# Optimization experiments

Hardware: AMD Instinct MI355X
Metric: run time of the kernel (lower is better)

The kernel has to match this reference:

```python
import jax, jax.numpy as jnp
import numpy as np

B, L, D, H = 2, 2048, 1024, 16
HD = D // H  # head_dim = 64


def setup_inputs() -> dict:
    key = jax.random.key(0)
    k1, k2, k3, k4, k5 = jax.random.split(key, 5)
    s = 1.0 / np.sqrt(D)
    return {
        "x": jax.random.normal(k1, (B, L, D), dtype=jnp.float32),
        "quantum_scores": jax.random.normal(k2, (B, L, L), dtype=jnp.float32),
        "wq": jax.random.normal(k3, (D, D), dtype=jnp.float32) * s,
        "wk": jax.random.normal(k4, (D, D), dtype=jnp.float32) * s,
        "wv": jax.random.normal(k5, (D, D), dtype=jnp.float32) * s,
        "scale": jnp.ones((H, 1, 1), dtype=jnp.float32),
    }


def reference(x, quantum_scores, wq, wk, wv, scale):
    Bq, Lq, _ = x.shape
    # nn.Linear: y = x @ W^T ; then split heads -> (B, H, L, HD)
    def split_heads(t):
        return t.reshape(Bq, Lq, H, HD).transpose(0, 2, 1, 3)

    q = split_heads(x @ wq.T)
    k = split_heads(x @ wk.T)
    v = split_heads(x @ wv.T)

    logits = jnp.einsum("bhqd,bhkd->bhqk", q, k) / np.sqrt(HD).astype(np.float32)
    logits = logits + quantum_scores[:, None, :, :]          # quantum bias, broadcast over heads
    logits = logits * scale[None, :, :, :]                   # per-head learnable scale
    attn = jax.nn.softmax(logits, axis=-1)
    out = jnp.einsum("bhqk,bhkd->bhqd", attn, v)
    return out.transpose(0, 2, 1, 3).reshape(Bq, Lq, D)
```

## Files before the change

### kernel.cpp

```cpp
#include <hip/hip_runtime.h>

#define Bq 2
#define Lq 2048
#define Dq 1024
#define Hq 16
#define HDq 64

typedef _Float16 f16;
typedef _Float16 f16x8 __attribute__((ext_vector_type(8)));
typedef _Float16 f16x4 __attribute__((ext_vector_type(4)));
typedef __fp16 hf16x2 __attribute__((ext_vector_type(2)));
typedef float f32x4 __attribute__((ext_vector_type(4)));
typedef float f32x16 __attribute__((ext_vector_type(16)));

__device__ __forceinline__ void gload_lds16(const void* g, void* l) {
    __builtin_amdgcn_global_load_lds(
        (const __attribute__((address_space(1))) unsigned int*)g,
        (__attribute__((address_space(3))) unsigned int*)l, 16, 0, 0);
}

__device__ __forceinline__ void swap32(int& a, int& b) {
    asm volatile("v_permlane32_swap_b32 %0, %1" : "+v"(a), "+v"(b));
}

__device__ __forceinline__ int pk2(float a, float b) {
    hf16x2 v = __builtin_amdgcn_cvt_pkrtz(a, b);
    return __builtin_bit_cast(int, v);
}

__global__ __launch_bounds__(256) void convert_kernel(
    const float* __restrict__ x,
    const float* __restrict__ wq, const float* __restrict__ wk, const float* __restrict__ wv,
    f16* __restrict__ x_h, f16* __restrict__ wq_h, f16* __restrict__ wk_h, f16* __restrict__ wv_h)
{
    const int NX = Bq*Lq*Dq;
    const int NW = Dq*Dq;
    const int total4 = (NX + 3*NW) / 4;
    for (int i = blockIdx.x*blockDim.x + threadIdx.x; i < total4;
         i += gridDim.x*blockDim.x) {
        int e = i * 4;
        const float* src; f16* dst; int off;
        if (e < NX) { src = x; dst = x_h; off = e; }
        else {
            int t = e - NX; int w = t >> 20; off = t & (NW-1);
            src = (w==0) ? wq : (w==1) ? wk : wv;
            dst = (w==0) ? wq_h : (w==1) ? wk_h : wv_h;
        }
        float4 v = *reinterpret_cast<const float4*>(src + off);
        f16x4 hv; hv.x=(f16)v.x; hv.y=(f16)v.y; hv.z=(f16)v.z; hv.w=(f16)v.w;
        *reinterpret_cast<f16x4*>(dst + off) = hv;
    }
}

#define GBM 128
#define GBN 128
#define GBK 32

__global__ __launch_bounds__(256) void qkv_mfma_kernel(
    const f16* __restrict__ x_h,
    const f16* __restrict__ wq_h, const f16* __restrict__ wk_h, const f16* __restrict__ wv_h,
    f16* __restrict__ q_h, f16* __restrict__ k_h, f16* __restrict__ vT_h)
{
    __shared__ __align__(16) f16 As[GBM*GBK];
    __shared__ __align__(16) f16 Bs[GBN*GBK];

    const int tid  = threadIdx.x;
    const int lane = tid & 63;
    const int wave = tid >> 6;
    const int wr = wave >> 1, wc = wave & 1;
    const int l15 = lane & 15, l4 = lane >> 4;
    const int n0 = blockIdx.x * GBN;
    const int m0 = blockIdx.y * GBM;
    const int z  = blockIdx.z;
    const f16* W = (z==0) ? wq_h : (z==1) ? wk_h : wv_h;

    const int sslot = tid & 3;

    f32x4 acc[4][4];
    #pragma unroll
    for (int i=0;i<4;++i)
        #pragma unroll
        for (int j=0;j<4;++j) acc[i][j] = f32x4{0.f,0.f,0.f,0.f};

    for (int kt = 0; kt < Dq; kt += GBK) {
        __syncthreads();
        #pragma unroll
        for (int j = 0; j < 2; ++j) {
            int slotIdx = tid + j*256;
            int row = slotIdx >> 2;
            gload_lds16(x_h + (size_t)(m0+row)*Dq + kt + sslot*8,
                        (char*)As + slotIdx*16);
            gload_lds16(W   + (size_t)(n0+row)*Dq + kt + sslot*8,
                        (char*)Bs + slotIdx*16);
        }
        __syncthreads();

        f16x8 a[4], b[4];
        #pragma unroll
        for (int m=0;m<4;++m) {
            int row = wr*64 + m*16 + l15;
            a[m] = *reinterpret_cast<const f16x8*>((const char*)As + row*64 + l4*16);
        }
        #pragma unroll
        for (int n=0;n<4;++n) {
            int row = wc*64 + n*16 + l15;
            b[n] = *reinterpret_cast<const f16x8*>((const char*)Bs + row*64 + l4*16);
        }
        #pragma unroll
        for (int m=0;m<4;++m)
            #pragma unroll
            for (int n=0;n<4;++n)
                acc[m][n] = __builtin_amdgcn_mfma_f32_16x16x32_f16(a[m], b[n], acc[m][n], 0,0,0);
    }

    #pragma unroll
    for (int m=0;m<4;++m) {
        #pragma unroll
        for (int r=0;r<4;++r) {
            int grow = m0 + wr*64 + m*16 + l4*4 + r;
            int b_   = grow >> 11;
            int lrow = grow & (Lq-1);
            #pragma unroll
            for (int n=0;n<4;++n) {
                int gcol = n0 + wc*64 + n*16 + l15;
                int h = gcol >> 6, d = gcol & 63;
                int bh = b_*Hq + h;
                f16 val = (f16)acc[m][n][r];
                if (z==0)      q_h[((size_t)bh*Lq + lrow)*HDq + d] = val;
                else if (z==1) k_h[((size_t)bh*Lq + lrow)*HDq + d] = val;
                else           vT_h[((size_t)bh*HDq + d)*Lq + lrow] = val;
            }
        }
    }
}

__global__ __launch_bounds__(256) void qm_pre_kernel(
    const float* __restrict__ quantum, f16* __restrict__ qm_pre)
{
    __shared__ float qs[32][64];
    const int tid = threadIdx.x;
    const int qt = blockIdx.x, kt = blockIdx.y, b = blockIdx.z;
    const float* base = quantum + ((size_t)b*Lq + qt*32)*Lq + kt*64;
    #pragma unroll
    for (int i=0;i<2;++i) {
        int idx = tid + i*256;
        int r = idx >> 4, c = (idx & 15)*4;
        float4 v = *reinterpret_cast<const float4*>(base + (size_t)r*Lq + c);
        qs[r][c]=v.x; qs[r][c+1]=v.y; qs[r][c+2]=v.z; qs[r][c+3]=v.w;
    }
    __syncthreads();
    const int seg = tid >> 6, lane = tid & 63, l31 = lane & 31, hi = lane >> 5;
    f16x8 u;
    #pragma unroll
    for (int e=0;e<8;++e) {
        int key = 16*seg + 8*(e>>2) + 4*hi + (e&3);
        u[e] = (f16)qs[l31][key];
    }
    f16* outp = qm_pre + (((size_t)b*32 + kt)*64 + qt)*2048 + seg*512 + lane*8;
    *reinterpret_cast<f16x8*>(outp) = u;
}

__global__ __launch_bounds__(256, 2) void attn4_kernel(
    const f16* __restrict__ q_h, const f16* __restrict__ k_h, const f16* __restrict__ vT_h,
    const f16* __restrict__ qm_pre, const float* __restrict__ scale,
    float* __restrict__ out)
{
    __shared__ __align__(16) char lds[49152];

    const int tid  = threadIdx.x;
    const int lane = tid & 63;
    const int wave = tid >> 6;
    const int l31  = lane & 31;
    const int hi   = lane >> 5;
    const int bh = blockIdx.x;
    const int qb = blockIdx.y;
    const int b_ = bh >> 4, h = bh & 15;
    const int qW = qb*128 + wave*32;
    const int qt = qb*4 + wave;
    const float sc = scale[h];
    const float c1 = 0.125f * sc * 1.44269504f;
    const float c2 = sc * 1.44269504f;

    const f16* kbase = k_h  + (size_t)bh*Lq*HDq;
    const f16* vbase = vT_h + (size_t)bh*HDq*Lq;

    f16x8 qf[4];
    {
        const f16* qb_ = q_h + ((size_t)bh*Lq + qW + l31)*HDq + hi*8;
        #pragma unroll
        for (int ds=0; ds<4; ++ds)
            qf[ds] = *reinterpret_cast<const f16x8*>(qb_ + ds*16);
    }

    f32x16 o0, o1;
    #pragma unroll
    for (int r=0;r<16;++r) { o0[r]=0.f; o1[r]=0.f; }
    float m_run = -1e30f, s_run = 0.f;

    auto STAGE = [&](int t, int buf) {
        const int k0 = t*64;
        char* LK = lds + buf*16384;
        char* LV = LK + 8192;
        #pragma unroll
        for (int i=0;i<2;++i) {
            int g = tid + i*256;
            int row = g >> 3, slot = g & 7;
            int ss = slot ^ (row & 7);
            gload_lds16(kbase + (size_t)(k0+row)*HDq + ss*8, LK + g*16);
            gload_lds16(vbase + (size_t)row*Lq + k0 + ss*8,  LV + g*16);
        }
    };

    auto QMLOAD = [&](int t, f16x8 (&qm)[4]) {
        const f16* qmb = qm_pre + (((size_t)b_*32 + t)*64 + qt)*2048 + lane*8;
        #pragma unroll
        for (int s=0;s<4;++s)
            qm[s] = *reinterpret_cast<const f16x8*>(qmb + s*512);
    };

    auto COMPUTE = [&](int t, int buf, f16x8 (&qmc)[4], f16x8 (&qmn)[4]) {
        const char* LK = lds + buf*16384;
        const char* LV = LK + 8192;
        int tn = (t+1 < 32) ? t+1 : 31;
        QMLOAD(tn, qmn);

        f32x16 st[2];
        __builtin_amdgcn_s_setprio(1);
        #pragma unroll
        for (int kt=0;kt<2;++kt) {
            #pragma unroll
            for (int r=0;r<16;++r) st[kt][r]=0.f;
            #pragma unroll
            for (int ds=0;ds<4;++ds) {
                f16x8 ka = *reinterpret_cast<const f16x8*>(
                    LK + ((kt*32+l31)<<7) + (((ds*2+hi)^(l31&7))<<4));
                st[kt] = __builtin_amdgcn_mfma_f32_32x32x16_f16(ka, qf[ds], st[kt], 0,0,0);
            }
        }
        __builtin_amdgcn_s_setprio(0);

        float lg[32];
        #pragma unroll
        for (int s=0;s<4;++s)
            #pragma unroll
            for (int e=0;e<8;++e) {
                int i = s*8 + e;
                float sv = (i < 16) ? st[0][i] : st[1][i-16];
                lg[i] = sv*c1 + (float)qmc[s][e]*c2;
            }

        float tm[16];
        #pragma unroll
        for (int r=0;r<16;++r) tm[r] = fmaxf(lg[r], lg[r+16]);
        #pragma unroll
        for (int w=8; w>0; w>>=1)
            #pragma unroll
            for (int r=0;r<w;++r) tm[r] = fmaxf(tm[r], tm[r+w]);
        float tmax = fmaxf(tm[0], __shfl_xor(tm[0], 32));

        if (!__all(tmax <= m_run + 8.f)) {
            float m_new = fmaxf(m_run, tmax);
            float corr = __builtin_amdgcn_exp2f(m_run - m_new);
            m_run = m_new;
            s_run *= corr;
            #pragma unroll
            for (int r=0;r<16;++r) { o0[r] *= corr; o1[r] *= corr; }
        }

        float p[32];
        #pragma unroll
        for (int r=0;r<32;++r) p[r] = __builtin_amdgcn_exp2f(lg[r] - m_run);
        float sm[16];
        #pragma unroll
        for (int r=0;r<16;++r) sm[r] = p[r] + p[r+16];
        #pragma unroll
        for (int w=8; w>0; w>>=1)
            #pragma unroll
            for (int r=0;r<w;++r) sm[r] += sm[r+w];
        s_run += sm[0];

        f16x8 pb[4];
        #pragma unroll
        for (int ks=0; ks<4; ++ks) {
            int w0 = pk2(p[8*ks+0], p[8*ks+1]);
            int w1 = pk2(p[8*ks+2], p[8*ks+3]);
            int w2 = pk2(p[8*ks+4], p[8*ks+5]);
            int w3 = pk2(p[8*ks+6], p[8*ks+7]);
            swap32(w0, w2);
            swap32(w1, w3);
            union { int w[4]; f16x8 v; } u;
            u.w[0]=w0; u.w[1]=w1; u.w[2]=w2; u.w[3]=w3;
            pb[ks] = u.v;
        }

        __builtin_amdgcn_s_setprio(1);
        #pragma unroll
        for (int ks=0; ks<4; ++ks) {
            f16x8 va0 = *reinterpret_cast<const f16x8*>(
                LV + (l31<<7)        + (((ks*2+hi)^(l31&7))<<4));
            f16x8 va1 = *reinterpret_cast<const f16x8*>(
                LV + ((32+l31)<<7)   + (((ks*2+hi)^(l31&7))<<4));
            o0 = __builtin_amdgcn_mfma_f32_32x32x16_f16(va0, pb[ks], o0, 0,0,0);
            o1 = __builtin_amdgcn_mfma_f32_32x32x16_f16(va1, pb[ks], o1, 0,0,0);
        }
        __builtin_amdgcn_s_setprio(0);
    };

    f16x8 qmE[4], qmO[4];

    QMLOAD(0, qmE);
    STAGE(0, 0);
    STAGE(1, 1);

    #define VMW(n) asm volatile("s_waitcnt vmcnt(" #n ")" ::: "memory")

    VMW(4);  __builtin_amdgcn_s_barrier();
    STAGE(2, 2);  COMPUTE(0, 0, qmE, qmO);
    VMW(8);  __builtin_amdgcn_s_barrier();
    STAGE(3, 0);  COMPUTE(1, 1, qmO, qmE);
    for (int t = 2; t < 30; t += 2) {
        VMW(12); __builtin_amdgcn_s_barrier();
        STAGE(t+2, (t+2)%3); COMPUTE(t, t%3, qmE, qmO);
        VMW(12); __builtin_amdgcn_s_barrier();
        STAGE(t+3, (t+3)%3); COMPUTE(t+1, (t+1)%3, qmO, qmE);
    }
    VMW(12); __builtin_amdgcn_s_barrier();
    COMPUTE(30, 0, qmE, qmO);
    VMW(8);  __builtin_amdgcn_s_barrier();
    COMPUTE(31, 1, qmO, qmE);

    #undef VMW

    float s_tot = s_run + __shfl_xor(s_run, 32);
    float inv = 1.0f / s_tot;
    float* ob = out + ((size_t)b_*Lq + qW + l31)*Dq + h*HDq;
    #pragma unroll
    for (int r=0;r<16;++r) {
        int drow = (r&3) + 8*(r>>2) + 4*hi;
        ob[drow]      = o0[r]*inv;
        ob[32 + drow] = o1[r]*inv;
    }
}

extern "C" void kernel_launch(void* const* d_in, const int* in_sizes, int n_in,
                              void* d_out, int out_size, void* d_ws, size_t ws_size,
                              hipStream_t stream) {
    const float* x       = (const float*)d_in[0];
    const float* quantum = (const float*)d_in[1];
    const float* wq      = (const float*)d_in[2];
    const float* wk      = (const float*)d_in[3];
    const float* wv      = (const float*)d_in[4];
    const float* scale   = (const float*)d_in[5];
    float* out = (float*)d_out;

    f16* ws     = (f16*)d_ws;
    f16* x_h    = ws;
    f16* wq_h   = ws + 4194304;
    f16* wk_h   = ws + 5242880;
    f16* wv_h   = ws + 6291456;
    f16* q_h    = ws + 7340032;
    f16* k_h    = ws + 11534336;
    f16* vT_h   = ws + 15728640;
    f16* qm_pre = ws + 19922944;

    convert_kernel<<<1024, 256, 0, stream>>>(x, wq, wk, wv, x_h, wq_h, wk_h, wv_h);

    dim3 gq(64, 32, 2);
    qm_pre_kernel<<<gq, 256, 0, stream>>>(quantum, qm_pre);

    dim3 g1(Dq/GBN, (Bq*Lq)/GBM, 3);
    qkv_mfma_kernel<<<g1, 256, 0, stream>>>(x_h, wq_h, wk_h, wv_h, q_h, k_h, vT_h);

    dim3 g2(Bq*Hq, Lq/128);
    attn4_kernel<<<g2, 256, 0, stream>>>(q_h, k_h, vT_h, qm_pre, scale, out);
}
```

Measured before the change: 130.7 us.

## Fold quantum bias into MFMA accumulator init and defer scaling into exp2

The bias is now pre-multiplied by 8 and stored as fp32 in the MFMA accumulator layout, so the QK^T MFMA starts from the bias instead of zero. The per-element logit scale-and-add pass goes away, and scaling is folded into the exp2 argument as one FMA. The running max is tracked on unscaled logits, with min/max chosen by the sign of the scale. The cost is double the bias traffic: fp32 instead of fp16, twice as many per-tile loads, and larger vmcnt waits. The fp32 bias also changes rounding compared with the fp16 path.

```diff
diff --git a/kernel.cpp b/kernel.cpp
--- a/kernel.cpp
+++ b/kernel.cpp
@@ -135,34 +135,37 @@
 }
 
 __global__ __launch_bounds__(256) void qm_pre_kernel(
-    const float* __restrict__ quantum, f16* __restrict__ qm_pre)
+    const float* __restrict__ quantum, float* __restrict__ qm_pre)
 {
-    __shared__ float qs[32][64];
+    __shared__ float qs[32][65];
     const int tid = threadIdx.x;
-    const int qt = blockIdx.x, kt = blockIdx.y, b = blockIdx.z;
-    const float* base = quantum + ((size_t)b*Lq + qt*32)*Lq + kt*64;
+    const int qt = blockIdx.x, t = blockIdx.y, b = blockIdx.z;
+    const float* base = quantum + ((size_t)b*Lq + qt*32)*Lq + t*64;
     #pragma unroll
     for (int i=0;i<2;++i) {
         int idx = tid + i*256;
         int r = idx >> 4, c = (idx & 15)*4;
         float4 v = *reinterpret_cast<const float4*>(base + (size_t)r*Lq + c);
-        qs[r][c]=v.x; qs[r][c+1]=v.y; qs[r][c+2]=v.z; qs[r][c+3]=v.w;
+        qs[r][c+0]=v.x*8.f; qs[r][c+1]=v.y*8.f; qs[r][c+2]=v.z*8.f; qs[r][c+3]=v.w*8.f;
     }
     __syncthreads();
-    const int seg = tid >> 6, lane = tid & 63, l31 = lane & 31, hi = lane >> 5;
-    f16x8 u;
-    #pragma unroll
-    for (int e=0;e<8;++e) {
-        int key = 16*seg + 8*(e>>2) + 4*hi + (e&3);
-        u[e] = (f16)qs[l31][key];
-    }
-    f16* outp = qm_pre + (((size_t)b*32 + kt)*64 + qt)*2048 + seg*512 + lane*8;
-    *reinterpret_cast<f16x8*>(outp) = u;
+    float* outb = qm_pre + (((size_t)b*32 + t)*64 + qt)*2048;
+    #pragma unroll
+    for (int i=0;i<2;++i) {
+        int g = tid + i*256;
+        int kt = g >> 8;
+        int j  = (g >> 6) & 3;
+        int lane = g & 63;
+        int l31 = lane & 31, hi = lane >> 5;
+        int col = kt*32 + 8*j + 4*hi;
+        float4 v = { qs[l31][col], qs[l31][col+1], qs[l31][col+2], qs[l31][col+3] };
+        *reinterpret_cast<float4*>(outb + ((size_t)kt*4 + j)*256 + lane*4) = v;
+    }
 }
 
 __global__ __launch_bounds__(256, 2) void attn4_kernel(
     const f16* __restrict__ q_h, const f16* __restrict__ k_h, const f16* __restrict__ vT_h,
-    const f16* __restrict__ qm_pre, const float* __restrict__ scale,
+    const float* __restrict__ qm_pre, const float* __restrict__ scale,
     float* __restrict__ out)
 {
     __shared__ __align__(16) char lds[49152];
@@ -177,9 +180,8 @@
     const int b_ = bh >> 4, h = bh & 15;
     const int qW = qb*128 + wave*32;
     const int qt = qb*4 + wave;
-    const float sc = scale[h];
-    const float c1 = 0.125f * sc * 1.44269504f;
-    const float c2 = sc * 1.44269504f;
+    const float c1 = 0.125f * scale[h] * 1.44269504f;
+    const bool pos = (c1 >= 0.f);
 
     const f16* kbase = k_h  + (size_t)bh*Lq*HDq;
     const f16* vbase = vT_h + (size_t)bh*HDq*Lq;
@@ -195,7 +197,8 @@
     f32x16 o0, o1;
     #pragma unroll
     for (int r=0;r<16;++r) { o0[r]=0.f; o1[r]=0.f; }
-    float m_run = -1e30f, s_run = 0.f;
+    float m_run = pos ? -1e30f : 1e30f;
+    float s_run = 0.f;
 
     auto STAGE = [&](int t, int buf) {
         const int k0 = t*64;
@@ -211,25 +214,32 @@
         }
     };
 
-    auto QMLOAD = [&](int t, f16x8 (&qm)[4]) {
-        const f16* qmb = qm_pre + (((size_t)b_*32 + t)*64 + qt)*2048 + lane*8;
-        #pragma unroll
-        for (int s=0;s<4;++s)
-            qm[s] = *reinterpret_cast<const f16x8*>(qmb + s*512);
+    auto QMLOAD = [&](int t, f32x4 (&qm)[2][4]) {
+        const char* qmb = (const char*)qm_pre
+            + ((((size_t)b_*32 + t)*64 + qt)*2048)*4 + lane*16;
+        #pragma unroll
+        for (int kt=0;kt<2;++kt)
+            #pragma unroll
+            for (int j=0;j<4;++j)
+                qm[kt][j] = *reinterpret_cast<const f32x4*>(qmb + kt*4096 + j*1024);
     };
 
-    auto COMPUTE = [&](int t, int buf, f16x8 (&qmc)[4], f16x8 (&qmn)[4]) {
+    auto COMPUTE = [&](int t, int buf, f32x4 (&qmc)[2][4], f32x4 (&qmn)[2][4]) {
         const char* LK = lds + buf*16384;
         const char* LV = LK + 8192;
         int tn = (t+1 < 32) ? t+1 : 31;
         QMLOAD(tn, qmn);
 
         f32x16 st[2];
+        #pragma unroll
+        for (int kt=0;kt<2;++kt)
+            #pragma unroll
+            for (int j=0;j<4;++j)
+                #pragma unroll
+                for (int c=0;c<4;++c) st[kt][4*j+c] = qmc[kt][j][c];
         __builtin_amdgcn_s_setprio(1);
         #pragma unroll
         for (int kt=0;kt<2;++kt) {
-            #pragma unroll
-            for (int r=0;r<16;++r) st[kt][r]=0.f;
             #pragma unroll
             for (int ds=0;ds<4;++ds) {
                 f16x8 ka = *reinterpret_cast<const f16x8*>(
@@ -239,37 +249,45 @@
         }
         __builtin_amdgcn_s_setprio(0);
 
-        float lg[32];
-        #pragma unroll
-        for (int s=0;s<4;++s)
-            #pragma unroll
-            for (int e=0;e<8;++e) {
-                int i = s*8 + e;
-                float sv = (i < 16) ? st[0][i] : st[1][i-16];
-                lg[i] = sv*c1 + (float)qmc[s][e]*c2;
+        float text;
+        {
+            float w_[16];
+            if (pos) {
+                #pragma unroll
+                for (int r=0;r<16;++r) w_[r] = fmaxf(st[0][r], st[1][r]);
+                #pragma unroll
+                for (int w=8; w>0; w>>=1)
+                    #pragma unroll
+                    for (int r=0;r<w;++r) w_[r] = fmaxf(w_[r], w_[r+w]);
+                text = fmaxf(w_[0], __shfl_xor(w_[0], 32));
+            } else {
+                #pragma unroll
+                for (int r=0;r<16;++r) w_[r] = fminf(st[0][r], st[1][r]);
+                #pragma unroll
+                for (int w=8; w>0; w>>=1)
+                    #pragma unroll
+                    for (int r=0;r<w;++r) w_[r] = fminf(w_[r], w_[r+w]);
+                text = fminf(w_[0], __shfl_xor(w_[0], 32));
             }
-
-        float tm[16];
-        #pragma unroll
-        for (int r=0;r<16;++r) tm[r] = fmaxf(lg[r], lg[r+16]);
-        #pragma unroll
-        for (int w=8; w>0; w>>=1)
-            #pragma unroll
-            for (int r=0;r<w;++r) tm[r] = fmaxf(tm[r], tm[r+w]);
-        float tmax = fmaxf(tm[0], __shfl_xor(tm[0], 32));
-
-        if (!__all(tmax <= m_run + 8.f)) {
-            float m_new = fmaxf(m_run, tmax);
-            float corr = __builtin_amdgcn_exp2f(m_run - m_new);
+        }
+
+        float u = c1*(text - m_run);
+        if (!__all(u <= 8.f)) {
+            float m_new = pos ? fmaxf(m_run, text) : fminf(m_run, text);
+            float corr = __builtin_amdgcn_exp2f(c1*(m_run - m_new));
             m_run = m_new;
             s_run *= corr;
             #pragma unroll
             for (int r=0;r<16;++r) { o0[r] *= corr; o1[r] *= corr; }
         }
 
+        float mb = c1 * m_run;
         float p[32];
         #pragma unroll
-        for (int r=0;r<32;++r) p[r] = __builtin_amdgcn_exp2f(lg[r] - m_run);
+        for (int r=0;r<16;++r) {
+            p[r]    = __builtin_amdgcn_exp2f(__builtin_fmaf(st[0][r], c1, -mb));
+            p[16+r] = __builtin_amdgcn_exp2f(__builtin_fmaf(st[1][r], c1, -mb));
+        }
         float sm[16];
         #pragma unroll
         for (int r=0;r<16;++r) sm[r] = p[r] + p[r+16];
@@ -288,9 +306,9 @@
             int w3 = pk2(p[8*ks+6], p[8*ks+7]);
             swap32(w0, w2);
             swap32(w1, w3);
-            union { int w[4]; f16x8 v; } u;
-            u.w[0]=w0; u.w[1]=w1; u.w[2]=w2; u.w[3]=w3;
-            pb[ks] = u.v;
+            union { int w[4]; f16x8 v; } u2;
+            u2.w[0]=w0; u2.w[1]=w1; u2.w[2]=w2; u2.w[3]=w3;
+            pb[ks] = u2.v;
         }
 
         __builtin_amdgcn_s_setprio(1);
@@ -306,7 +324,7 @@
         __builtin_amdgcn_s_setprio(0);
     };
 
-    f16x8 qmE[4], qmO[4];
+    f32x4 qmE[2][4], qmO[2][4];
 
     QMLOAD(0, qmE);
     STAGE(0, 0);
@@ -316,17 +334,17 @@
 
     VMW(4);  __builtin_amdgcn_s_barrier();
     STAGE(2, 2);  COMPUTE(0, 0, qmE, qmO);
-    VMW(8);  __builtin_amdgcn_s_barrier();
+    VMW(12); __builtin_amdgcn_s_barrier();
     STAGE(3, 0);  COMPUTE(1, 1, qmO, qmE);
     for (int t = 2; t < 30; t += 2) {
-        VMW(12); __builtin_amdgcn_s_barrier();
+        VMW(20); __builtin_amdgcn_s_barrier();
         STAGE(t+2, (t+2)%3); COMPUTE(t, t%3, qmE, qmO);
-        VMW(12); __builtin_amdgcn_s_barrier();
+        VMW(20); __builtin_amdgcn_s_barrier();
         STAGE(t+3, (t+3)%3); COMPUTE(t+1, (t+1)%3, qmO, qmE);
     }
-    VMW(12); __builtin_amdgcn_s_barrier();
+    VMW(20); __builtin_amdgcn_s_barrier();
     COMPUTE(30, 0, qmE, qmO);
-    VMW(8);  __builtin_amdgcn_s_barrier();
+    VMW(16); __builtin_amdgcn_s_barrier();
     COMPUTE(31, 1, qmO, qmE);
 
     #undef VMW
@@ -361,16 +379,16 @@
     f16* q_h    = ws + 7340032;
     f16* k_h    = ws + 11534336;
     f16* vT_h   = ws + 15728640;
-    f16* qm_pre = ws + 19922944;
+    float* qm32 = (float*)(ws + 19922944);
 
     convert_kernel<<<1024, 256, 0, stream>>>(x, wq, wk, wv, x_h, wq_h, wk_h, wv_h);
 
     dim3 gq(64, 32, 2);
-    qm_pre_kernel<<<gq, 256, 0, stream>>>(quantum, qm_pre);
+    qm_pre_kernel<<<gq, 256, 0, stream>>>(quantum, qm32);
 
     dim3 g1(Dq/GBN, (Bq*Lq)/GBM, 3);
     qkv_mfma_kernel<<<g1, 256, 0, stream>>>(x_h, wq_h, wk_h, wv_h, q_h, k_h, vT_h);
 
     dim3 g2(Bq*Hq, Lq/128);
-    attn4_kernel<<<g2, 256, 0, stream>>>(q_h, k_h, vT_h, qm_pre, scale, out);
-}
+    attn4_kernel<<<g2, 256, 0, stream>>>(q_h, k_h, vT_h, qm32, scale, out);
+}
```

Measured after the change: 134.8 us. 1.03x slower.

## Merge QKV GEMM with bias preprocessing launch and pair-step attention pipeline

Applied to the files above, without the earlier changes.

The QKV projection GEMM and the quantum-bias fp16 relayout are merged into one launch by splitting the block index range, so the bias conversion blocks can run alongside the GEMM blocks and one launch is removed. Separately, the attention kernel's LDS grows from three to four K/V stage buffers, and the loop now stages two tiles and computes two tiles per barrier. This halves the number of barriers and waits per sweep but uses more LDS per block, which may lower occupancy given the two-blocks-per-CU launch bound.

```diff
diff --git a/kernel.cpp b/kernel.cpp
--- a/kernel.cpp
+++ b/kernel.cpp
@@ -56,108 +56,111 @@
 #define GBN 128
 #define GBK 32
 
-__global__ __launch_bounds__(256) void qkv_mfma_kernel(
+__global__ __launch_bounds__(256) void qkv_qm_fused_kernel(
     const f16* __restrict__ x_h,
     const f16* __restrict__ wq_h, const f16* __restrict__ wk_h, const f16* __restrict__ wv_h,
-    f16* __restrict__ q_h, f16* __restrict__ k_h, f16* __restrict__ vT_h)
+    const float* __restrict__ quantum,
+    f16* __restrict__ q_h, f16* __restrict__ k_h, f16* __restrict__ vT_h,
+    f16* __restrict__ qm_pre)
 {
-    __shared__ __align__(16) f16 As[GBM*GBK];
-    __shared__ __align__(16) f16 Bs[GBN*GBK];
-
-    const int tid  = threadIdx.x;
-    const int lane = tid & 63;
-    const int wave = tid >> 6;
-    const int wr = wave >> 1, wc = wave & 1;
-    const int l15 = lane & 15, l4 = lane >> 4;
-    const int n0 = blockIdx.x * GBN;
-    const int m0 = blockIdx.y * GBM;
-    const int z  = blockIdx.z;
-    const f16* W = (z==0) ? wq_h : (z==1) ? wk_h : wv_h;
-
-    const int sslot = tid & 3;
-
-    f32x4 acc[4][4];
-    #pragma unroll
-    for (int i=0;i<4;++i)
-        #pragma unroll
-        for (int j=0;j<4;++j) acc[i][j] = f32x4{0.f,0.f,0.f,0.f};
-
-    for (int kt = 0; kt < Dq; kt += GBK) {
+    __shared__ __align__(16) char smem[16384];
+    const int tid = threadIdx.x;
+    const int id  = blockIdx.x;
+
+    if (id < 768) {
+        f16* As = (f16*)smem;
+        f16* Bs = (f16*)(smem + 8192);
+        const int lane = tid & 63;
+        const int wave = tid >> 6;
+        const int wr = wave >> 1, wc = wave & 1;
+        const int l15 = lane & 15, l4 = lane >> 4;
+        const int n0 = (id & 7) * GBN;
+        const int m0 = ((id >> 3) & 31) * GBM;
+        const int z  = id >> 8;
+        const f16* W = (z==0) ? wq_h : (z==1) ? wk_h : wv_h;
+        const int sslot = tid & 3;
+
+        f32x4 acc[4][4];
+        #pragma unroll
+        for (int i=0;i<4;++i)
+            #pragma unroll
+            for (int j=0;j<4;++j) acc[i][j] = f32x4{0.f,0.f,0.f,0.f};
+
+        for (int kt = 0; kt < Dq; kt += GBK) {
+            __syncthreads();
+            #pragma unroll
+            for (int j = 0; j < 2; ++j) {
+                int slotIdx = tid + j*256;
+                int row = slotIdx >> 2;
+                gload_lds16(x_h + (size_t)(m0+row)*Dq + kt + sslot*8,
+                            (char*)As + slotIdx*16);
+                gload_lds16(W   + (size_t)(n0+row)*Dq + kt + sslot*8,
+                            (char*)Bs + slotIdx*16);
+            }
+            __syncthreads();
+
+            f16x8 a[4], b[4];
+            #pragma unroll
+            for (int m=0;m<4;++m) {
+                int row = wr*64 + m*16 + l15;
+                a[m] = *reinterpret_cast<const f16x8*>((const char*)As + row*64 + l4*16);
+            }
+            #pragma unroll
+            for (int n=0;n<4;++n) {
+                int row = wc*64 + n*16 + l15;
+                b[n] = *reinterpret_cast<const f16x8*>((const char*)Bs + row*64 + l4*16);
+            }
+            #pragma unroll
+            for (int m=0;m<4;++m)
+                #pragma unroll
+                for (int n=0;n<4;++n)
+                    acc[m][n] = __builtin_amdgcn_mfma_f32_16x16x32_f16(a[m], b[n], acc[m][n], 0,0,0);
+        }
+
+        #pragma unroll
+        for (int m=0;m<4;++m) {
+            #pragma unroll
+            for (int r=0;r<4;++r) {
+                int grow = m0 + wr*64 + m*16 + l4*4 + r;
+                int b_   = grow >> 11;
+                int lrow = grow & (Lq-1);
+                #pragma unroll
+                for (int n=0;n<4;++n) {
+                    int gcol = n0 + wc*64 + n*16 + l15;
+                    int h = gcol >> 6, d = gcol & 63;
+                    int bh = b_*Hq + h;
+                    f16 val = (f16)acc[m][n][r];
+                    if (z==0)      q_h[((size_t)bh*Lq + lrow)*HDq + d] = val;
+                    else if (z==1) k_h[((size_t)bh*Lq + lrow)*HDq + d] = val;
+                    else           vT_h[((size_t)bh*HDq + d)*Lq + lrow] = val;
+                }
+            }
+        }
+    } else {
+        float (*qs)[64] = (float(*)[64])smem;
+        const int q  = id - 768;
+        const int qt = q & 63;
+        const int kt = (q >> 6) & 31;
+        const int b  = q >> 11;
+        const float* base = quantum + ((size_t)b*Lq + qt*32)*Lq + kt*64;
+        #pragma unroll
+        for (int i=0;i<2;++i) {
+            int idx = tid + i*256;
+            int r = idx >> 4, c = (idx & 15)*4;
+            float4 v = *reinterpret_cast<const float4*>(base + (size_t)r*Lq + c);
+            qs[r][c]=v.x; qs[r][c+1]=v.y; qs[r][c+2]=v.z; qs[r][c+3]=v.w;
+        }
         __syncthreads();
-        #pragma unroll
-        for (int j = 0; j < 2; ++j) {
-            int slotIdx = tid + j*256;
-            int row = slotIdx >> 2;
-            gload_lds16(x_h + (size_t)(m0+row)*Dq + kt + sslot*8,
-                        (char*)As + slotIdx*16);
-            gload_lds16(W   + (size_t)(n0+row)*Dq + kt + sslot*8,
-                        (char*)Bs + slotIdx*16);
-        }
-        __syncthreads();
-
-        f16x8 a[4], b[4];
-        #pragma unroll
-        for (int m=0;m<4;++m) {
-            int row = wr*64 + m*16 + l15;
-            a[m] = *reinterpret_cast<const f16x8*>((const char*)As + row*64 + l4*16);
-        }
-        #pragma unroll
-        for (int n=0;n<4;++n) {
-            int row = wc*64 + n*16 + l15;
-            b[n] = *reinterpret_cast<const f16x8*>((const char*)Bs + row*64 + l4*16);
-        }
-        #pragma unroll
-        for (int m=0;m<4;++m)
-            #pragma unroll
-            for (int n=0;n<4;++n)
-                acc[m][n] = __builtin_amdgcn_mfma_f32_16x16x32_f16(a[m], b[n], acc[m][n], 0,0,0);
-    }
-
-    #pragma unroll
-    for (int m=0;m<4;++m) {
-        #pragma unroll
-        for (int r=0;r<4;++r) {
-            int grow = m0 + wr*64 + m*16 + l4*4 + r;
-            int b_   = grow >> 11;
-            int lrow = grow & (Lq-1);
-            #pragma unroll
-            for (int n=0;n<4;++n) {
-                int gcol = n0 + wc*64 + n*16 + l15;
-                int h = gcol >> 6, d = gcol & 63;
-                int bh = b_*Hq + h;
-                f16 val = (f16)acc[m][n][r];
-                if (z==0)      q_h[((size_t)bh*Lq + lrow)*HDq + d] = val;
-                else if (z==1) k_h[((size_t)bh*Lq + lrow)*HDq + d] = val;
-                else           vT_h[((size_t)bh*HDq + d)*Lq + lrow] = val;
-            }
-        }
-    }
-}
-
-__global__ __launch_bounds__(256) void qm_pre_kernel(
-    const float* __restrict__ quantum, f16* __restrict__ qm_pre)
-{
-    __shared__ float qs[32][64];
-    const int tid = threadIdx.x;
-    const int qt = blockIdx.x, kt = blockIdx.y, b = blockIdx.z;
-    const float* base = quantum + ((size_t)b*Lq + qt*32)*Lq + kt*64;
-    #pragma unroll
-    for (int i=0;i<2;++i) {
-        int idx = tid + i*256;
-        int r = idx >> 4, c = (idx & 15)*4;
-        float4 v = *reinterpret_cast<const float4*>(base + (size_t)r*Lq + c);
-        qs[r][c]=v.x; qs[r][c+1]=v.y; qs[r][c+2]=v.z; qs[r][c+3]=v.w;
-    }
-    __syncthreads();
-    const int seg = tid >> 6, lane = tid & 63, l31 = lane & 31, hi = lane >> 5;
-    f16x8 u;
-    #pragma unroll
-    for (int e=0;e<8;++e) {
-        int key = 16*seg + 8*(e>>2) + 4*hi + (e&3);
-        u[e] = (f16)qs[l31][key];
-    }
-    f16* outp = qm_pre + (((size_t)b*32 + kt)*64 + qt)*2048 + seg*512 + lane*8;
-    *reinterpret_cast<f16x8*>(outp) = u;
+        const int seg = tid >> 6, lane = tid & 63, l31 = lane & 31, hi = lane >> 5;
+        f16x8 u;
+        #pragma unroll
+        for (int e=0;e<8;++e) {
+            int key = 16*seg + 8*(e>>2) + 4*hi + (e&3);
+            u[e] = (f16)qs[l31][key];
+        }
+        f16* outp = qm_pre + (((size_t)b*32 + kt)*64 + qt)*2048 + seg*512 + lane*8;
+        *reinterpret_cast<f16x8*>(outp) = u;
+    }
 }
 
 __global__ __launch_bounds__(256, 2) void attn4_kernel(
@@ -165,7 +168,7 @@
     const f16* __restrict__ qm_pre, const float* __restrict__ scale,
     float* __restrict__ out)
 {
-    __shared__ __align__(16) char lds[49152];
+    __shared__ __align__(16) char lds[65536];
 
     const int tid  = threadIdx.x;
     const int lane = tid & 63;
@@ -197,9 +200,11 @@
     for (int r=0;r<16;++r) { o0[r]=0.f; o1[r]=0.f; }
     float m_run = -1e30f, s_run = 0.f;
 
-    auto STAGE = [&](int t, int buf) {
+    auto QTR = [](int t) { return ((t >> 1) & 1)*2 + (t & 1); };
+
+    auto STAGE = [&](int t) {
         const int k0 = t*64;
-        char* LK = lds + buf*16384;
+        char* LK = lds + QTR(t)*16384;
         char* LV = LK + 8192;
         #pragma unroll
         for (int i=0;i<2;++i) {
@@ -218,8 +223,8 @@
             qm[s] = *reinterpret_cast<const f16x8*>(qmb + s*512);
     };
 
-    auto COMPUTE = [&](int t, int buf, f16x8 (&qmc)[4], f16x8 (&qmn)[4]) {
-        const char* LK = lds + buf*16384;
+    auto COMPUTE = [&](int t, f16x8 (&qmc)[4], f16x8 (&qmn)[4]) {
+        const char* LK = lds + QTR(t)*16384;
         const char* LV = LK + 8192;
         int tn = (t+1 < 32) ? t+1 : 31;
         QMLOAD(tn, qmn);
@@ -309,25 +314,23 @@
     f16x8 qmE[4], qmO[4];
 
     QMLOAD(0, qmE);
-    STAGE(0, 0);
-    STAGE(1, 1);
+    STAGE(0); STAGE(1);
 
     #define VMW(n) asm volatile("s_waitcnt vmcnt(" #n ")" ::: "memory")
 
-    VMW(4);  __builtin_amdgcn_s_barrier();
-    STAGE(2, 2);  COMPUTE(0, 0, qmE, qmO);
-    VMW(8);  __builtin_amdgcn_s_barrier();
-    STAGE(3, 0);  COMPUTE(1, 1, qmO, qmE);
-    for (int t = 2; t < 30; t += 2) {
-        VMW(12); __builtin_amdgcn_s_barrier();
-        STAGE(t+2, (t+2)%3); COMPUTE(t, t%3, qmE, qmO);
-        VMW(12); __builtin_amdgcn_s_barrier();
-        STAGE(t+3, (t+3)%3); COMPUTE(t+1, (t+1)%3, qmO, qmE);
-    }
-    VMW(12); __builtin_amdgcn_s_barrier();
-    COMPUTE(30, 0, qmE, qmO);
-    VMW(8);  __builtin_amdgcn_s_barrier();
-    COMPUTE(31, 1, qmO, qmE);
+    VMW(0); __builtin_amdgcn_s_barrier();
+    STAGE(2); STAGE(3);
+    COMPUTE(0, qmE, qmO);
+    COMPUTE(1, qmO, qmE);
+    for (int e = 1; e < 15; ++e) {
+        VMW(8); __builtin_amdgcn_s_barrier();
+        STAGE(2*e+2); STAGE(2*e+3);
+        COMPUTE(2*e,   qmE, qmO);
+        COMPUTE(2*e+1, qmO, qmE);
+    }
+    VMW(8); __builtin_amdgcn_s_barrier();
+    COMPUTE(30, qmE, qmO);
+    COMPUTE(31, qmO, qmE);
 
     #undef VMW
 
@@ -365,11 +368,8 @@
 
     convert_kernel<<<1024, 256, 0, stream>>>(x, wq, wk, wv, x_h, wq_h, wk_h, wv_h);
 
-    dim3 gq(64, 32, 2);
-    qm_pre_kernel<<<gq, 256, 0, stream>>>(quantum, qm_pre);
-
-    dim3 g1(Dq/GBN, (Bq*Lq)/GBM, 3);
-    qkv_mfma_kernel<<<g1, 256, 0, stream>>>(x_h, wq_h, wk_h, wv_h, q_h, k_h, vT_h);
+    qkv_qm_fused_kernel<<<4864, 256, 0, stream>>>(
+        x_h, wq_h, wk_h, wv_h, quantum, q_h, k_h, vT_h, qm_pre);
 
     dim3 g2(Bq*Hq, Lq/128);
     attn4_kernel<<<g2, 256, 0, stream>>>(q_h, k_h, vT_h, qm_pre, scale, out);
```

New measurement: 127.1 us. 2.7% less time.
